# Performance work log

Hardware: AMD Instinct MI355X
Metric: run time of the kernel (lower is better)

The kernel has to match this reference:

```python
import jax, jax.numpy as jnp
import numpy as np


def setup_inputs() -> dict:
    key = jax.random.key(0)
    kx, kw = jax.random.split(key)
    batch, n_in, n_out = 8192, 4096, 4096
    x = jax.random.normal(kx, (batch, n_in), dtype=jnp.float32)
    stdv = 1.0 / np.sqrt(n_in)
    w = jax.random.normal(kw, (n_in, n_out), dtype=jnp.float32) * stdv
    return {"x": x, "w": w}


def reference(x, w):
    # fp16_grad forward: fp32 -> fp16 -> fp32 round trip on weights
    w16 = w.astype(jnp.float16).astype(jnp.float32)
    # binarize_weight forward: sign(clip(w, -1, 1))  (STE only affects backward)
    wb = jnp.sign(jnp.clip(w16, -1.0, 1.0))
    # dense matmul with binarized weights: [B, n_in] @ [n_in, n_out]
    return x @ wb
```

## Files before the change

### kernel.cpp

```cpp
#include <hip/hip_runtime.h>
#include <hip/hip_fp16.h>

#define MM 8192
#define NN 4096
#define KK 4096
#define BM 256
#define BN 256
#define BK 64
#define NT (KK / BK)

typedef __attribute__((ext_vector_type(8))) short bf16x8;
typedef __attribute__((ext_vector_type(4))) float floatx4;
typedef __attribute__((ext_vector_type(8))) unsigned short ushort8_t;

typedef const __attribute__((address_space(1))) unsigned int* gptr_t;
typedef __attribute__((address_space(3))) unsigned int* lptr_t;

__device__ __forceinline__ unsigned short f2bf(float f) {
    unsigned u = __builtin_bit_cast(unsigned, f);
    u += 0x7FFFu + ((u >> 16) & 1u);
    return (unsigned short)(u >> 16);
}

__device__ __forceinline__ unsigned short sign_bf16(float f) {
    float h = __half2float(__float2half(f));
    return (h > 0.f) ? 0x3F80u : ((h < 0.f) ? 0xBF80u : 0u);
}

__global__ __launch_bounds__(256) void cvt_x_kernel(const float4* __restrict__ x4,
                                                    ushort8_t* __restrict__ o8, int n8) {
    int i = blockIdx.x * 256 + threadIdx.x;
    if (i >= n8) return;
    float4 a = x4[2 * i];
    float4 b = x4[2 * i + 1];
    ushort8_t o;
    o[0] = f2bf(a.x); o[1] = f2bf(a.y); o[2] = f2bf(a.z); o[3] = f2bf(a.w);
    o[4] = f2bf(b.x); o[5] = f2bf(b.y); o[6] = f2bf(b.z); o[7] = f2bf(b.w);
    o8[i] = o;
}

__global__ __launch_bounds__(256) void binz_wt_kernel(const float* __restrict__ w,
                                                      unsigned short* __restrict__ wt) {
    __shared__ unsigned short tileT[64][72];
    const int n0 = blockIdx.x * 64;
    const int k0 = blockIdx.y * 64;
    const int t  = threadIdx.x;
    {
        const int c4 = t & 15;
        const int rb = t >> 4;
#pragma unroll
        for (int i = 0; i < 4; ++i) {
            int r = rb + i * 16;
            float4 v = *(const float4*)&w[(size_t)(k0 + r) * NN + n0 + c4 * 4];
            tileT[c4 * 4 + 0][r] = sign_bf16(v.x);
            tileT[c4 * 4 + 1][r] = sign_bf16(v.y);
            tileT[c4 * 4 + 2][r] = sign_bf16(v.z);
            tileT[c4 * 4 + 3][r] = sign_bf16(v.w);
        }
    }
    __syncthreads();
    {
        const int g  = t & 7;
        const int nb = t >> 3;
#pragma unroll
        for (int i = 0; i < 2; ++i) {
            int n = nb + i * 32;
            *(ushort8_t*)&wt[(size_t)(n0 + n) * KK + k0 + g * 8] =
                *(const ushort8_t*)&tileT[n][g * 8];
        }
    }
}

__global__ __launch_bounds__(512, 2) void gemm_bin_kernel(const unsigned short* __restrict__ A,
                                                          const unsigned short* __restrict__ Bt,
                                                          float* __restrict__ C) {
    __shared__ __align__(16) char lds[131072];

    const int tid    = threadIdx.x;
    const int lane   = tid & 63;
    const int wave   = tid >> 6;
    const int wave_u = __builtin_amdgcn_readfirstlane(wave);
    const int wm     = wave >> 2;
    const int wn     = wave & 3;
    const int l15    = lane & 15;
    const int kq     = lane >> 4;

    const int bid = blockIdx.x;
    const int wg  = (bid & 7) * 64 + (bid >> 3);
    const int bn0 = (wg & 15) * BN;
    const int bm0 = (wg >> 4) * BM;

    const int r0 = tid >> 3;
    const int c0 = (tid & 7) ^ (r0 & 7);
    const char* gA = (const char*)A;
    const char* gB = (const char*)Bt;
    const size_t aoff = (size_t)(bm0 + r0) * (KK * 2) + (size_t)c0 * 16;
    const size_t boff = (size_t)(bn0 + r0) * (KK * 2) + (size_t)c0 * 16;

    __attribute__((address_space(3))) char* lds3 =
        (__attribute__((address_space(3))) char*)lds;
    const int dstw = wave_u * 1024;

    const int aco0 = ((0 * 4 + kq) ^ (lane & 7)) * 16;
    const int aco1 = ((1 * 4 + kq) ^ (lane & 7)) * 16;
    const char* ldsA_l = lds + l15 * 128;
    const char* ldsB_l = lds + 65536 + ((wn & 1) * 64 + l15) * 128;
    const char* pA0 = ldsA_l + (0 * 2 + wm) * 16384;
    const char* pA1 = ldsA_l + (1 * 2 + wm) * 16384;
    const char* pB0 = ldsB_l + (0 * 2 + (wn >> 1)) * 16384;
    const char* pB1 = ldsB_l + (1 * 2 + (wn >> 1)) * 16384;

    floatx4 acc[8][4] = {};
    bf16x8 af[8][2];
    bf16x8 bfr[4][2];

    auto STAGE_A = [&](int h, int kt) {
        const int slot = (kt & 1) * 2 + h;
        const char* s0 = gA + aoff + (size_t)h * (128 * KK * 2) + (size_t)kt * (BK * 2);
        __builtin_amdgcn_global_load_lds((gptr_t)s0,
            (lptr_t)(lds3 + slot * 16384 + dstw), 16, 0, 0);
        __builtin_amdgcn_global_load_lds((gptr_t)(s0 + (size_t)64 * KK * 2),
            (lptr_t)(lds3 + slot * 16384 + 8192 + dstw), 16, 0, 0);
    };
    auto STAGE_B = [&](int h, int kt) {
        const int slot = (kt & 1) * 2 + h;
        const char* s0 = gB + boff + (size_t)h * (128 * KK * 2) + (size_t)kt * (BK * 2);
        __builtin_amdgcn_global_load_lds((gptr_t)s0,
            (lptr_t)(lds3 + 65536 + slot * 16384 + dstw), 16, 0, 0);
        __builtin_amdgcn_global_load_lds((gptr_t)(s0 + (size_t)64 * KK * 2),
            (lptr_t)(lds3 + 65536 + slot * 16384 + 8192 + dstw), 16, 0, 0);
    };
    auto LDA = [&](const char* pAp, int mf) {
        af[mf][0] = *(const bf16x8*)(pAp + aco0 + mf * 2048);
        af[mf][1] = *(const bf16x8*)(pAp + aco1 + mf * 2048);
    };
    auto LDB = [&](const char* pBp, int nf) {
        bfr[nf][0] = *(const bf16x8*)(pBp + aco0 + nf * 2048);
        bfr[nf][1] = *(const bf16x8*)(pBp + aco1 + nf * 2048);
    };
    auto QUAD8 = [&](int mb, int nb) {
#pragma unroll
        for (int mi = 0; mi < 4; ++mi)
#pragma unroll
            for (int nj = 0; nj < 2; ++nj)
#pragma unroll
                for (int ks = 0; ks < 2; ++ks)
                    acc[mb + mi][nb + nj] = __builtin_amdgcn_mfma_f32_16x16x32_bf16(
                        af[mb + mi][ks], bfr[nb + nj][ks], acc[mb + mi][nb + nj], 0, 0, 0);
    };

#define WAITL(n) do { asm volatile("s_waitcnt lgkmcnt(" #n ")" ::: "memory"); \
                      __builtin_amdgcn_sched_barrier(0); } while (0)

    STAGE_B(0, 0); STAGE_B(1, 0); STAGE_A(0, 0); STAGE_A(1, 0);
    STAGE_B(0, 1); STAGE_B(1, 1); STAGE_A(0, 1);
    asm volatile("s_waitcnt vmcnt(6)" ::: "memory");
    __builtin_amdgcn_s_barrier();
    LDA(pA0, 0); LDA(pA0, 1); LDA(pA0, 2); LDA(pA0, 3);
    LDB(pB0, 0); LDB(pB0, 1);

#define TILE_BODY(t, pAc, pBc, pAn, pBn)                                        \
    {                                                                           \
                                   \
        LDA(pAc, 4); LDA(pAc, 5); LDA(pAc, 6); LDA(pAc, 7);                     \
        if ((t) + 1 < NT) STAGE_A(1, (t) + 1);                                  \
        __builtin_amdgcn_s_barrier();                                           \
        WAITL(8);                                                               \
        __builtin_amdgcn_s_setprio(1);                                          \
        QUAD8(0, 0);                                                            \
        __builtin_amdgcn_s_setprio(0);                                          \
        __builtin_amdgcn_s_barrier();                                           \
                                  \
        LDB(pBc, 2); LDB(pBc, 3);                                               \
        if ((t) + 2 < NT) STAGE_B(0, (t) + 2);                                  \
        __builtin_amdgcn_s_barrier();                                           \
        WAITL(4);                                                               \
        __builtin_amdgcn_s_setprio(1);                                          \
        QUAD8(4, 0);                                                            \
        __builtin_amdgcn_s_setprio(0);                                          \
        __builtin_amdgcn_s_barrier();                                           \
                        \
        WAITL(0);                                                               \
        __builtin_amdgcn_s_setprio(1);                                          \
        QUAD8(0, 2);                                                            \
        __builtin_amdgcn_s_setprio(0);                                          \
        __builtin_amdgcn_s_barrier();                                           \
         \
        if ((t) + 2 < NT) { STAGE_B(1, (t) + 2); STAGE_A(0, (t) + 2); }         \
        if ((t) == NT - 2) { asm volatile("s_waitcnt vmcnt(0)" ::: "memory"); } \
        else               { asm volatile("s_waitcnt vmcnt(6)" ::: "memory"); } \
        __builtin_amdgcn_s_barrier();                                           \
        LDA(pAn, 0); LDA(pAn, 1); LDA(pAn, 2); LDA(pAn, 3);                     \
        LDB(pBn, 0); LDB(pBn, 1);                                               \
        WAITL(12);                                                              \
        __builtin_amdgcn_s_setprio(1);                                          \
        QUAD8(4, 2);                                                            \
        __builtin_amdgcn_s_setprio(0);                                          \
        __builtin_amdgcn_s_barrier();                                           \
    }

    for (int tb = 0; tb < NT; tb += 2) {
        TILE_BODY(tb,     pA0, pB0, pA1, pB1);
        TILE_BODY(tb + 1, pA1, pB1, pA0, pB0);
    }
#undef TILE_BODY
#undef WAITL

#pragma unroll
    for (int mf = 0; mf < 8; ++mf) {
#pragma unroll
        for (int nf = 0; nf < 4; ++nf) {
            const size_t row = (size_t)(bm0 + wm * 128 + mf * 16 + kq * 4);
            const int col = bn0 + wn * 64 + nf * 16 + l15;
#pragma unroll
            for (int r = 0; r < 4; ++r)
                C[(row + r) * NN + col] = acc[mf][nf][r];
        }
    }
}

__global__ __launch_bounds__(256) void fallback_kernel(const float* __restrict__ x,
                                                       const float* __restrict__ w,
                                                       float* __restrict__ out) {
    int n = blockIdx.x * 256 + threadIdx.x;
    int m = blockIdx.y;
    float s = 0.f;
    for (int k = 0; k < KK; ++k) {
        float h = __half2float(__float2half(w[(size_t)k * NN + n]));
        float b = (h > 0.f) ? 1.f : ((h < 0.f) ? -1.f : 0.f);
        s += x[(size_t)m * KK + k] * b;
    }
    out[(size_t)m * NN + n] = s;
}

extern "C" void kernel_launch(void* const* d_in, const int* in_sizes, int n_in,
                              void* d_out, int out_size, void* d_ws, size_t ws_size,
                              hipStream_t stream) {
    const float* x = (const float*)d_in[0];
    const float* w = (const float*)d_in[1];
    if (n_in >= 2 && in_sizes[0] != MM * KK) {
        x = (const float*)d_in[1];
        w = (const float*)d_in[0];
    }
    float* out = (float*)d_out;

    const size_t xb_bytes = (size_t)MM * KK * 2;
    const size_t wt_bytes = (size_t)NN * KK * 2;

    if (ws_size >= xb_bytes + wt_bytes) {
        unsigned short* xb = (unsigned short*)d_ws;
        unsigned short* wt = (unsigned short*)((char*)d_ws + xb_bytes);

        int n8 = MM * KK / 8;
        cvt_x_kernel<<<(n8 + 255) / 256, 256, 0, stream>>>((const float4*)x, (ushort8_t*)xb, n8);
        binz_wt_kernel<<<dim3(NN / 64, KK / 64), 256, 0, stream>>>(w, wt);
        gemm_bin_kernel<<<dim3((NN / BN) * (MM / BM)), dim3(512), 0, stream>>>(xb, wt, out);
    } else {
        fallback_kernel<<<dim3(NN / 256, MM), 256, 0, stream>>>(x, w, out);
    }
}
```

Measured before the change: 468.0 us.

## Switch GEMM to 32x32x16 bf16 MFMA tiles and restructure pipeline

The GEMM inner loop moves from 16x16x32 MFMA fragments to 32x32x16 MFMA with 16-wide accumulators. This changes the LDS fragment addressing, the per-wave register layout and the epilogue store mapping. The tile body is reorganised into four MFMA phases that wait for LDS loads with full lgkmcnt(0), dropping the cross-tile prefetch of the next tile's fragments. The x conversion kernel now handles two float4 per thread at strided offsets. Larger MFMAs cut instruction and LDS-read overhead, but the full waits may expose more LDS latency.

Result: slower. 512.2 us (+9.4%).

```diff
diff --git a/kernel.cpp b/kernel.cpp
--- a/kernel.cpp
+++ b/kernel.cpp
@@ -10,7 +10,7 @@
 #define NT (KK / BK)
 
 typedef __attribute__((ext_vector_type(8))) short bf16x8;
-typedef __attribute__((ext_vector_type(4))) float floatx4;
+typedef __attribute__((ext_vector_type(16))) float floatx16;
 typedef __attribute__((ext_vector_type(8))) unsigned short ushort8_t;
 
 typedef const __attribute__((address_space(1))) unsigned int* gptr_t;
@@ -28,15 +28,16 @@
 }
 
 __global__ __launch_bounds__(256) void cvt_x_kernel(const float4* __restrict__ x4,
-                                                    ushort8_t* __restrict__ o8, int n8) {
-    int i = blockIdx.x * 256 + threadIdx.x;
-    if (i >= n8) return;
-    float4 a = x4[2 * i];
-    float4 b = x4[2 * i + 1];
-    ushort8_t o;
-    o[0] = f2bf(a.x); o[1] = f2bf(a.y); o[2] = f2bf(a.z); o[3] = f2bf(a.w);
-    o[4] = f2bf(b.x); o[5] = f2bf(b.y); o[6] = f2bf(b.z); o[7] = f2bf(b.w);
-    o8[i] = o;
+                                                    ushort4* __restrict__ o4) {
+    int i0 = blockIdx.x * 512 + threadIdx.x;
+    int i1 = i0 + 256;
+    float4 a = x4[i0];
+    float4 b = x4[i1];
+    ushort4 oa, ob;
+    oa.x = f2bf(a.x); oa.y = f2bf(a.y); oa.z = f2bf(a.z); oa.w = f2bf(a.w);
+    ob.x = f2bf(b.x); ob.y = f2bf(b.y); ob.z = f2bf(b.z); ob.w = f2bf(b.w);
+    o4[i0] = oa;
+    o4[i1] = ob;
 }
 
 __global__ __launch_bounds__(256) void binz_wt_kernel(const float* __restrict__ w,
@@ -82,8 +83,8 @@
     const int wave_u = __builtin_amdgcn_readfirstlane(wave);
     const int wm     = wave >> 2;
     const int wn     = wave & 3;
-    const int l15    = lane & 15;
-    const int kq     = lane >> 4;
+    const int l31    = lane & 31;
+    const int kh     = lane >> 5;
 
     const int bid = blockIdx.x;
     const int wg  = (bid & 7) * 64 + (bid >> 3);
@@ -101,18 +102,20 @@
         (__attribute__((address_space(3))) char*)lds;
     const int dstw = wave_u * 1024;
 
-    const int aco0 = ((0 * 4 + kq) ^ (lane & 7)) * 16;
-    const int aco1 = ((1 * 4 + kq) ^ (lane & 7)) * 16;
-    const char* ldsA_l = lds + l15 * 128;
-    const char* ldsB_l = lds + 65536 + ((wn & 1) * 64 + l15) * 128;
+    const int aco0 = ((0 * 2 + kh) ^ (lane & 7)) * 16;
+    const int aco1 = ((1 * 2 + kh) ^ (lane & 7)) * 16;
+    const int aco2 = ((2 * 2 + kh) ^ (lane & 7)) * 16;
+    const int aco3 = ((3 * 2 + kh) ^ (lane & 7)) * 16;
+    const char* ldsA_l = lds + l31 * 128;
+    const char* ldsB_l = lds + 65536 + ((wn & 1) * 64 + l31) * 128;
     const char* pA0 = ldsA_l + (0 * 2 + wm) * 16384;
     const char* pA1 = ldsA_l + (1 * 2 + wm) * 16384;
     const char* pB0 = ldsB_l + (0 * 2 + (wn >> 1)) * 16384;
     const char* pB1 = ldsB_l + (1 * 2 + (wn >> 1)) * 16384;
 
-    floatx4 acc[8][4] = {};
-    bf16x8 af[8][2];
-    bf16x8 bfr[4][2];
+    floatx16 acc[4][2] = {};
+    bf16x8 af[4][4];
+    bf16x8 bf[2][4];
 
     auto STAGE_A = [&](int h, int kt) {
         const int slot = (kt & 1) * 2 + h;
@@ -131,90 +134,90 @@
             (lptr_t)(lds3 + 65536 + slot * 16384 + 8192 + dstw), 16, 0, 0);
     };
     auto LDA = [&](const char* pAp, int mf) {
-        af[mf][0] = *(const bf16x8*)(pAp + aco0 + mf * 2048);
-        af[mf][1] = *(const bf16x8*)(pAp + aco1 + mf * 2048);
+        af[mf][0] = *(const bf16x8*)(pAp + mf * 4096 + aco0);
+        af[mf][1] = *(const bf16x8*)(pAp + mf * 4096 + aco1);
+        af[mf][2] = *(const bf16x8*)(pAp + mf * 4096 + aco2);
+        af[mf][3] = *(const bf16x8*)(pAp + mf * 4096 + aco3);
     };
     auto LDB = [&](const char* pBp, int nf) {
-        bfr[nf][0] = *(const bf16x8*)(pBp + aco0 + nf * 2048);
-        bfr[nf][1] = *(const bf16x8*)(pBp + aco1 + nf * 2048);
-    };
-    auto QUAD8 = [&](int mb, int nb) {
-#pragma unroll
-        for (int mi = 0; mi < 4; ++mi)
-#pragma unroll
-            for (int nj = 0; nj < 2; ++nj)
-#pragma unroll
-                for (int ks = 0; ks < 2; ++ks)
-                    acc[mb + mi][nb + nj] = __builtin_amdgcn_mfma_f32_16x16x32_bf16(
-                        af[mb + mi][ks], bfr[nb + nj][ks], acc[mb + mi][nb + nj], 0, 0, 0);
-    };
-
-#define WAITL(n) do { asm volatile("s_waitcnt lgkmcnt(" #n ")" ::: "memory"); \
-                      __builtin_amdgcn_sched_barrier(0); } while (0)
+        bf[nf][0] = *(const bf16x8*)(pBp + nf * 4096 + aco0);
+        bf[nf][1] = *(const bf16x8*)(pBp + nf * 4096 + aco1);
+        bf[nf][2] = *(const bf16x8*)(pBp + nf * 4096 + aco2);
+        bf[nf][3] = *(const bf16x8*)(pBp + nf * 4096 + aco3);
+    };
+    auto MFMA8 = [&](int mh, int nf) {
+#pragma unroll
+        for (int mi = 0; mi < 2; ++mi)
+#pragma unroll
+            for (int kf = 0; kf < 4; ++kf)
+                acc[2 * mh + mi][nf] = __builtin_amdgcn_mfma_f32_32x32x16_bf16(
+                    af[2 * mh + mi][kf], bf[nf][kf], acc[2 * mh + mi][nf], 0, 0, 0);
+    };
+
+#define WAITL0 do { asm volatile("s_waitcnt lgkmcnt(0)" ::: "memory"); \
+                    __builtin_amdgcn_sched_barrier(0); } while (0)
 
     STAGE_B(0, 0); STAGE_B(1, 0); STAGE_A(0, 0); STAGE_A(1, 0);
-    STAGE_B(0, 1); STAGE_B(1, 1); STAGE_A(0, 1);
+    STAGE_B(1, 1); STAGE_A(0, 1); STAGE_B(0, 1);
     asm volatile("s_waitcnt vmcnt(6)" ::: "memory");
     __builtin_amdgcn_s_barrier();
-    LDA(pA0, 0); LDA(pA0, 1); LDA(pA0, 2); LDA(pA0, 3);
-    LDB(pB0, 0); LDB(pB0, 1);
-
-#define TILE_BODY(t, pAc, pBc, pAn, pBn)                                        \
+
+#define TILE_BODY(t, pAc, pBc)                                                  \
     {                                                                           \
-                                   \
-        LDA(pAc, 4); LDA(pAc, 5); LDA(pAc, 6); LDA(pAc, 7);                     \
+                        \
+        LDA(pAc, 0); LDA(pAc, 1); LDB(pBc, 0);                                  \
         if ((t) + 1 < NT) STAGE_A(1, (t) + 1);                                  \
         __builtin_amdgcn_s_barrier();                                           \
-        WAITL(8);                                                               \
-        __builtin_amdgcn_s_setprio(1);                                          \
-        QUAD8(0, 0);                                                            \
-        __builtin_amdgcn_s_setprio(0);                                          \
-        __builtin_amdgcn_s_barrier();                                           \
-                                  \
-        LDB(pBc, 2); LDB(pBc, 3);                                               \
-        if ((t) + 2 < NT) STAGE_B(0, (t) + 2);                                  \
-        __builtin_amdgcn_s_barrier();                                           \
-        WAITL(4);                                                               \
-        __builtin_amdgcn_s_setprio(1);                                          \
-        QUAD8(4, 0);                                                            \
-        __builtin_amdgcn_s_setprio(0);                                          \
-        __builtin_amdgcn_s_barrier();                                           \
-                        \
-        WAITL(0);                                                               \
-        __builtin_amdgcn_s_setprio(1);                                          \
-        QUAD8(0, 2);                                                            \
-        __builtin_amdgcn_s_setprio(0);                                          \
-        __builtin_amdgcn_s_barrier();                                           \
-         \
-        if ((t) + 2 < NT) { STAGE_B(1, (t) + 2); STAGE_A(0, (t) + 2); }         \
+        WAITL0;                                                                 \
+        __builtin_amdgcn_s_setprio(1);                                          \
+        MFMA8(0, 0);                                                            \
+        __builtin_amdgcn_s_setprio(0);                                          \
+        __builtin_amdgcn_s_barrier();                                           \
+                                             \
+        LDA(pAc, 2); LDA(pAc, 3);                                               \
+        __builtin_amdgcn_s_barrier();                                           \
+        WAITL0;                                                                 \
+        __builtin_amdgcn_s_setprio(1);                                          \
+        MFMA8(1, 0);                                                            \
+        __builtin_amdgcn_s_setprio(0);                                          \
+        __builtin_amdgcn_s_barrier();                                           \
+                                               \
+        LDB(pBc, 1);                                                            \
+        __builtin_amdgcn_s_barrier();                                           \
+        WAITL0;                                                                 \
+        __builtin_amdgcn_s_setprio(1);                                          \
+        MFMA8(0, 1);                                                            \
+        __builtin_amdgcn_s_setprio(0);                                          \
+        __builtin_amdgcn_s_barrier();                                           \
+          \
+        if ((t) + 2 < NT) { STAGE_B(1, (t) + 2); STAGE_A(0, (t) + 2);           \
+                            STAGE_B(0, (t) + 2); }                              \
+        __builtin_amdgcn_s_setprio(1);                                          \
+        MFMA8(1, 1);                                                            \
+        __builtin_amdgcn_s_setprio(0);                                          \
         if ((t) == NT - 2) { asm volatile("s_waitcnt vmcnt(0)" ::: "memory"); } \
         else               { asm volatile("s_waitcnt vmcnt(6)" ::: "memory"); } \
         __builtin_amdgcn_s_barrier();                                           \
-        LDA(pAn, 0); LDA(pAn, 1); LDA(pAn, 2); LDA(pAn, 3);                     \
-        LDB(pBn, 0); LDB(pBn, 1);                                               \
-        WAITL(12);                                                              \
-        __builtin_amdgcn_s_setprio(1);                                          \
-        QUAD8(4, 2);                                                            \
-        __builtin_amdgcn_s_setprio(0);                                          \
-        __builtin_amdgcn_s_barrier();                                           \
     }
 
     for (int tb = 0; tb < NT; tb += 2) {
-        TILE_BODY(tb,     pA0, pB0, pA1, pB1);
-        TILE_BODY(tb + 1, pA1, pB1, pA0, pB0);
+        TILE_BODY(tb,     pA0, pB0);
+        TILE_BODY(tb + 1, pA1, pB1);
     }
 #undef TILE_BODY
-#undef WAITL
-
-#pragma unroll
-    for (int mf = 0; mf < 8; ++mf) {
-#pragma unroll
-        for (int nf = 0; nf < 4; ++nf) {
-            const size_t row = (size_t)(bm0 + wm * 128 + mf * 16 + kq * 4);
-            const int col = bn0 + wn * 64 + nf * 16 + l15;
-#pragma unroll
-            for (int r = 0; r < 4; ++r)
-                C[(row + r) * NN + col] = acc[mf][nf][r];
+#undef WAITL0
+
+#pragma unroll
+    for (int mf = 0; mf < 4; ++mf) {
+#pragma unroll
+        for (int nf = 0; nf < 2; ++nf) {
+            const int rbase = bm0 + wm * 128 + mf * 32 + 4 * kh;
+            const int col   = bn0 + wn * 64 + nf * 32 + l31;
+#pragma unroll
+            for (int r = 0; r < 16; ++r) {
+                int row = rbase + (r & 3) + 8 * (r >> 2);
+                C[(size_t)row * NN + col] = acc[mf][nf][r];
+            }
         }
     }
 }
@@ -251,8 +254,8 @@
         unsigned short* xb = (unsigned short*)d_ws;
         unsigned short* wt = (unsigned short*)((char*)d_ws + xb_bytes);
 
-        int n8 = MM * KK / 8;
-        cvt_x_kernel<<<(n8 + 255) / 256, 256, 0, stream>>>((const float4*)x, (ushort8_t*)xb, n8);
+        int nblk = MM * KK / 4 / 512;
+        cvt_x_kernel<<<nblk, 256, 0, stream>>>((const float4*)x, (ushort4*)xb);
         binz_wt_kernel<<<dim3(NN / 64, KK / 64), 256, 0, stream>>>(w, wt);
         gemm_bin_kernel<<<dim3((NN / BN) * (MM / BM)), dim3(512), 0, stream>>>(xb, wt, out);
     } else {
```
